# Performance work log

Hardware: AMD Instinct MI355X
Metric: run time of the kernel (lower is better)

Reference implementation:

```python
import jax, jax.numpy as jnp
import numpy as np

B, T, D = 4, 2048, 1024  # batch, seq, latent_dim == attn_dim
H = 16                   # n_heads
HS = D // H              # head_size = 64
FF = 4 * D               # ffn hidden
EPS = 1e-5


def layernorm(x, g, b):
    mu = jnp.mean(x, axis=-1, keepdims=True)
    var = jnp.mean(jnp.square(x - mu), axis=-1, keepdims=True)
    return (x - mu) * jax.lax.rsqrt(var + EPS) * g + b


def setup_inputs() -> dict:
    key = jax.random.key(0)
    ks = jax.random.split(key, 12)
    s = lambda fan_in: 1.0 / np.sqrt(fan_in)
    return {
        "x": jax.random.normal(ks[0], (B, T, D), dtype=jnp.float32),
        "ln1_g": jnp.ones((D,), jnp.float32),
        "ln1_b": jnp.zeros((D,), jnp.float32),
        "W_ap": jax.random.normal(ks[1], (D, D), jnp.float32) * s(D),
        "b_ap": jnp.zeros((D,), jnp.float32),
        "W_qkv": jax.random.normal(ks[2], (D, 3 * D), jnp.float32) * s(D),
        "b_qkv": jnp.zeros((3 * D,), jnp.float32),
        "W_proj": jax.random.normal(ks[3], (D, D), jnp.float32) * s(D),
        "b_proj": jnp.zeros((D,), jnp.float32),
        "ln2_g": jnp.ones((D,), jnp.float32),
        "ln2_b": jnp.zeros((D,), jnp.float32),
        "W1": jax.random.normal(ks[4], (D, FF), jnp.float32) * s(D),
        "b1": jnp.zeros((FF,), jnp.float32),
        "W2": jax.random.normal(ks[5], (FF, D), jnp.float32) * s(FF),
        "b2": jnp.zeros((D,), jnp.float32),
    }


def block_fwd(x, ln1_g, ln1_b, W_ap, b_ap, W_qkv, b_qkv, W_proj, b_proj,
              ln2_g, ln2_b, W1, b1, W2, b2):
    # --- self attention branch ---
    a = layernorm(x, ln1_g, ln1_b)
    a = a @ W_ap + b_ap                       # [B,T,D]
    qkv = a @ W_qkv + b_qkv                   # [B,T,3D]
    q, k, v = jnp.split(qkv, 3, axis=-1)
    q = q.reshape(B, T, H, HS).transpose(0, 2, 1, 3)  # [B,H,T,HS]
    k = k.reshape(B, T, H, HS).transpose(0, 2, 1, 3)
    v = v.reshape(B, T, H, HS).transpose(0, 2, 1, 3)
    scores = jnp.einsum('bhqd,bhkd->bhqk', q, k) * (1.0 / np.sqrt(HS))
    probs = jax.nn.softmax(scores, axis=-1)   # full [B,H,T,T], no causal mask (as in source)
    o = jnp.einsum('bhqk,bhkd->bhqd', probs, v)
    o = o.transpose(0, 2, 1, 3).reshape(B, T, D)
    o = o @ W_proj + b_proj
    h = x + o
    # --- ffn branch: GELU(LayerNorm(h)) -> Linear -> GELU -> Linear ---
    f = jax.nn.gelu(layernorm(h, ln2_g, ln2_b), approximate=False)
    f = jax.nn.gelu(f @ W1 + b1, approximate=False) @ W2 + b2
    return h + f


def reference(x, ln1_g, ln1_b, W_ap, b_ap, W_qkv, b_qkv, W_proj, b_proj,
              ln2_g, ln2_b, W1, b1, W2, b2):
    return block_fwd(x, ln1_g, ln1_b, W_ap, b_ap, W_qkv, b_qkv, W_proj, b_proj,
                     ln2_g, ln2_b, W1, b1, W2, b2)
```

## Files before the change

kernel.cpp:

```cpp
#include <hip/hip_runtime.h>
#include <hip/hip_bf16.h>
#include <math.h>


typedef unsigned short u16;
typedef __attribute__((ext_vector_type(8))) short s16x8;
typedef __attribute__((ext_vector_type(4))) float f32x4;

__device__ __forceinline__ u16 f2bf(float f) {
    unsigned u = __float_as_uint(f);
    u += 0x7fffu + ((u >> 16) & 1u);
    return (u16)(u >> 16);
}
__device__ __forceinline__ unsigned pkbf2(float a, float b) {
    float2 t; t.x = a; t.y = b;
    __hip_bfloat162 r = __float22bfloat162_rn(t);
    return *(unsigned*)&r;
}
__device__ __forceinline__ float bf2f(short s) {
    return __uint_as_float(((unsigned)(unsigned short)s) << 16);
}
__device__ __forceinline__ float gelu_f(float v) {
    float u = v * v;
    float x = v * fmaf(0.0356774081f, u, 0.7978845608f);
    float t = __builtin_amdgcn_exp2f(x * 2.885390082f);
    float th = fmaf(-2.0f, __builtin_amdgcn_rcpf(t + 1.0f), 1.0f);
    float hv = 0.5f * v;
    return fmaf(hv, th, hv);
}
__device__ __forceinline__ void glds16(const u16* g, u16* l) {
    __builtin_amdgcn_global_load_lds(
        (const __attribute__((address_space(1))) void*)g,
        (__attribute__((address_space(3))) void*)l, 16, 0, 0);
}
__device__ __forceinline__ void barfence() {
    __builtin_amdgcn_s_barrier();
    asm volatile("" ::: "memory");
}

__global__ __launch_bounds__(256) void transpose_f32_bf16(
    const float* __restrict__ in, u16* __restrict__ out, int K, int N) {
    __shared__ float t[32][33];
    int n0 = blockIdx.x * 32, k0 = blockIdx.y * 32;
    int c = threadIdx.x, r0 = threadIdx.y;
#pragma unroll
    for (int i = 0; i < 4; i++) {
        int r = r0 + i * 8;
        t[r][c] = in[(size_t)(k0 + r) * N + n0 + c];
    }
    __syncthreads();
#pragma unroll
    for (int i = 0; i < 4; i++) {
        int r = r0 + i * 8;
        out[(size_t)(n0 + r) * K + k0 + c] = f2bf(t[c][r]);
    }
}

template <bool GELU>
__global__ __launch_bounds__(256) void ln_kernel(
    const float* __restrict__ x, const float* __restrict__ g,
    const float* __restrict__ bt, u16* __restrict__ out) {
    const int D = 1024;
    int row = blockIdx.x;
    float4 v = reinterpret_cast<const float4*>(x + (size_t)row * D)[threadIdx.x];
    float s = v.x + v.y + v.z + v.w;
    float s2 = v.x * v.x + v.y * v.y + v.z * v.z + v.w * v.w;
#pragma unroll
    for (int off = 32; off > 0; off >>= 1) {
        s += __shfl_down(s, off);
        s2 += __shfl_down(s2, off);
    }
    __shared__ float red[8];
    int wid = threadIdx.x >> 6;
    if ((threadIdx.x & 63) == 0) { red[wid] = s; red[wid + 4] = s2; }
    __syncthreads();
    s = red[0] + red[1] + red[2] + red[3];
    s2 = red[4] + red[5] + red[6] + red[7];
    float mu = s * (1.0f / 1024.0f);
    float var = s2 * (1.0f / 1024.0f) - mu * mu;
    float rstd = rsqrtf(var + 1e-5f);
    float4 gg = reinterpret_cast<const float4*>(g)[threadIdx.x];
    float4 bb = reinterpret_cast<const float4*>(bt)[threadIdx.x];
    float o0 = (v.x - mu) * rstd * gg.x + bb.x;
    float o1 = (v.y - mu) * rstd * gg.y + bb.y;
    float o2 = (v.z - mu) * rstd * gg.z + bb.z;
    float o3 = (v.w - mu) * rstd * gg.w + bb.w;
    if (GELU) { o0 = gelu_f(o0); o1 = gelu_f(o1); o2 = gelu_f(o2); o3 = gelu_f(o3); }
    uint2 o;
    o.x = pkbf2(o0, o1); o.y = pkbf2(o2, o3);
    reinterpret_cast<uint2*>(out + (size_t)row * D)[threadIdx.x] = o;
}

template <int OUT_BF16, int ACT_GELU, int HAS_RES>
__global__ __launch_bounds__(512, 2) void gemm_kernel(
    const u16* __restrict__ A, const u16* __restrict__ BT,
    const float* __restrict__ bias, const float* __restrict__ res,
    void* __restrict__ outp, int M, int N, int K) {
    __shared__ u16 As[2 * 256 * 64];
    __shared__ u16 Bs[2 * 256 * 64];
    const int nwg = gridDim.x * gridDim.y;
    int wg = blockIdx.y * gridDim.x + blockIdx.x;
    wg = (wg & 7) * (nwg >> 3) + (wg >> 3);
    const int m0 = (wg / gridDim.x) * 256, n0 = (wg % gridDim.x) * 256;
    const int tid = threadIdx.x;
    const int w = tid >> 6, lane = tid & 63, l16 = lane & 15, quad = lane >> 4;
    const int wm = w >> 2, wn = w & 3;

    const int lrow = lane >> 3;
    const int lcol = ((lane & 7) ^ lrow) * 8;
    const u16* Ag = A + (size_t)(m0 + w * 16 + lrow) * K + lcol;
    const u16* Bg = BT + (size_t)(n0 + w * 16 + lrow) * K + lcol;

    const int cx0 = (quad ^ (l16 & 7)) * 8;
    const int cx1 = cx0 ^ 32;

    f32x4 acc[2][2][4][2] = {};
    const int nt = K >> 6;

#define STAGE_A(AH, BUF, KK)                                              \
    do {                                                                  \
        const u16* _s = Ag + (size_t)((AH) * 128) * K + (KK);             \
        u16* _d = As + (BUF) * 16384 + ((AH) * 128 + w * 16) * 64;        \
        glds16(_s, _d);                                                   \
        glds16(_s + (size_t)8 * K, _d + 512);                             \
    } while (0)
#define STAGE_B(BH, BUF, KK)                                              \
    do {                                                                  \
        const u16* _s = Bg + (size_t)((BH) * 128) * K + (KK);             \
        u16* _d = Bs + (BUF) * 16384 + ((BH) * 128 + w * 16) * 64;        \
        glds16(_s, _d);                                                   \
        glds16(_s + (size_t)8 * K, _d + 512);                             \
    } while (0)

    STAGE_A(0, 0, 0);
    STAGE_B(0, 0, 0);
    STAGE_B(1, 0, 0);
    STAGE_A(1, 0, 0);
    asm volatile("s_waitcnt vmcnt(0)" ::: "memory");
    barfence();

    s16x8 af0[4][2], af1[4][2], bfA[2][2], bfB[2][2];

    for (int t = 0; t < nt; ++t) {
        const int cur = t & 1, nxt = cur ^ 1;
        const int kk = (t + 1) << 6;
        const bool pre = (t + 1) < nt;
        const u16* Ab = As + cur * 16384;
        const u16* Bb = Bs + cur * 16384;

#pragma unroll
        for (int j = 0; j < 2; ++j) {
            const u16* p = Bb + (wn * 32 + j * 16 + l16) * 64;
            bfA[j][0] = *(const s16x8*)(p + cx0);
            bfA[j][1] = *(const s16x8*)(p + cx1);
        }
#pragma unroll
        for (int i = 0; i < 4; ++i) {
            const u16* p = Ab + (wm * 64 + i * 16 + l16) * 64;
            af0[i][0] = *(const s16x8*)(p + cx0);
            af0[i][1] = *(const s16x8*)(p + cx1);
        }
#pragma unroll
        for (int j = 0; j < 2; ++j) {
            const u16* p = Bb + (128 + wn * 32 + j * 16 + l16) * 64;
            bfB[j][0] = *(const s16x8*)(p + cx0);
            bfB[j][1] = *(const s16x8*)(p + cx1);
        }
#pragma unroll
        for (int i = 0; i < 4; ++i) {
            const u16* p = Ab + (128 + wm * 64 + i * 16 + l16) * 64;
            af1[i][0] = *(const s16x8*)(p + cx0);
            af1[i][1] = *(const s16x8*)(p + cx1);
        }
        if (pre) {
            STAGE_A(0, nxt, kk);
            STAGE_B(0, nxt, kk);
            STAGE_B(1, nxt, kk);
            STAGE_A(1, nxt, kk);
        }
        __builtin_amdgcn_s_setprio(1);
#pragma unroll
        for (int kd = 0; kd < 2; ++kd)
#pragma unroll
            for (int i = 0; i < 4; ++i)
#pragma unroll
                for (int j = 0; j < 2; ++j)
                    acc[0][0][i][j] = __builtin_amdgcn_mfma_f32_16x16x32_bf16(
                        af0[i][kd], bfA[j][kd], acc[0][0][i][j], 0, 0, 0);
#pragma unroll
        for (int kd = 0; kd < 2; ++kd)
#pragma unroll
            for (int i = 0; i < 4; ++i)
#pragma unroll
                for (int j = 0; j < 2; ++j)
                    acc[0][1][i][j] = __builtin_amdgcn_mfma_f32_16x16x32_bf16(
                        af0[i][kd], bfB[j][kd], acc[0][1][i][j], 0, 0, 0);
#pragma unroll
        for (int kd = 0; kd < 2; ++kd)
#pragma unroll
            for (int i = 0; i < 4; ++i)
#pragma unroll
                for (int j = 0; j < 2; ++j)
                    acc[1][1][i][j] = __builtin_amdgcn_mfma_f32_16x16x32_bf16(
                        af1[i][kd], bfB[j][kd], acc[1][1][i][j], 0, 0, 0);
#pragma unroll
        for (int kd = 0; kd < 2; ++kd)
#pragma unroll
            for (int i = 0; i < 4; ++i)
#pragma unroll
                for (int j = 0; j < 2; ++j)
                    acc[1][0][i][j] = __builtin_amdgcn_mfma_f32_16x16x32_bf16(
                        af1[i][kd], bfA[j][kd], acc[1][0][i][j], 0, 0, 0);
        __builtin_amdgcn_s_setprio(0);
        if (pre) {
            asm volatile("s_waitcnt vmcnt(0)" ::: "memory");
            barfence();
        }
    }
#undef STAGE_A
#undef STAGE_B

    float bv[2][2];
#pragma unroll
    for (int bh = 0; bh < 2; ++bh)
#pragma unroll
        for (int j = 0; j < 2; ++j)
            bv[bh][j] = bias[n0 + bh * 128 + wn * 32 + j * 16 + l16];

#pragma unroll
    for (int ah = 0; ah < 2; ++ah)
#pragma unroll
        for (int i = 0; i < 4; ++i) {
            int rowb = m0 + ah * 128 + wm * 64 + i * 16 + quad * 4;
#pragma unroll
            for (int bh = 0; bh < 2; ++bh)
#pragma unroll
                for (int j = 0; j < 2; ++j) {
                    int col = n0 + bh * 128 + wn * 32 + j * 16 + l16;
#pragma unroll
                    for (int r = 0; r < 4; ++r) {
                        float v = acc[ah][bh][i][j][r] + bv[bh][j];
                        if (ACT_GELU) v = gelu_f(v);
                        size_t idx = (size_t)(rowb + r) * N + col;
                        if (HAS_RES) v += res[idx];
                        if (OUT_BF16) ((u16*)outp)[idx] = f2bf(v);
                        else          ((float*)outp)[idx] = v;
                    }
                }
        }
}

template <int OUT_BF16, int HAS_RES, int SPLIT_V>
__global__ __launch_bounds__(512, 2) void gemm_n128(
    const u16* __restrict__ A, const u16* __restrict__ BT,
    const float* __restrict__ bias, const float* __restrict__ res,
    void* __restrict__ outp, u16* __restrict__ vtg, int M, int N, int K) {
    __shared__ u16 As[3 * 256 * 64];
    __shared__ u16 Bs[3 * 128 * 64];
    const int nwg = gridDim.x * gridDim.y;
    int wg = blockIdx.y * gridDim.x + blockIdx.x;
    wg = (wg & 7) * (nwg >> 3) + (wg >> 3);
    const int m0 = (wg / gridDim.x) * 256, n0 = (wg % gridDim.x) * 128;
    const int tid = threadIdx.x;
    const int w = tid >> 6, lane = tid & 63, l16 = lane & 15, quad = lane >> 4;
    const int wm = w >> 1, wn = w & 1;

    const int lrow = lane >> 3;
    const int lcol = ((lane & 7) ^ lrow) * 8;
    const u16* Ag = A + (size_t)(m0 + w * 16 + lrow) * K + lcol;
    const u16* Bg = BT + (size_t)(n0 + w * 16 + lrow) * K + lcol;

    const int cx0 = (quad ^ (l16 & 7)) * 8;
    const int cx1 = cx0 ^ 32;

    f32x4 acc[4][4] = {};
    const int nt = K >> 6;

#define NSTAGE_A(BUF, KK)                                                 \
    do {                                                                  \
        const u16* _s = Ag + (KK);                                        \
        u16* _d = As + (BUF) * 16384 + (w * 16) * 64;                     \
        glds16(_s, _d);                                                   \
        glds16(_s + (size_t)8 * K, _d + 512);                             \
        glds16(_s + (size_t)128 * K, _d + 8192);                          \
        glds16(_s + (size_t)136 * K, _d + 8192 + 512);                    \
    } while (0)
#define NSTAGE_B(BUF, KK)                                                 \
    do {                                                                  \
        const u16* _s = Bg + (KK);                                        \
        u16* _d = Bs + (BUF) * 8192 + (w * 16) * 64;                      \
        glds16(_s, _d);                                                   \
        glds16(_s + (size_t)8 * K, _d + 512);                             \
    } while (0)

    NSTAGE_A(0, 0);
    NSTAGE_B(0, 0);
    NSTAGE_A(1, 64);
    NSTAGE_B(1, 64);
    asm volatile("s_waitcnt vmcnt(6)" ::: "memory");
    barfence();

    s16x8 af[4][2], bfA[2][2], bfB[2][2];
    int cur = 0, b2 = 2;
    for (int t = 0; t < nt; ++t) {
        const bool pre2 = (t + 2) < nt;
        const u16* Ab = As + cur * 16384;
        const u16* Bb = Bs + cur * 8192;
        const int kk2 = (t + 2) << 6;

#pragma unroll
        for (int j = 0; j < 2; ++j) {
            const u16* p = Bb + (wn * 64 + j * 16 + l16) * 64;
            bfA[j][0] = *(const s16x8*)(p + cx0);
            bfA[j][1] = *(const s16x8*)(p + cx1);
        }
#pragma unroll
        for (int i = 0; i < 4; ++i) {
            const u16* p = Ab + (wm * 64 + i * 16 + l16) * 64;
            af[i][0] = *(const s16x8*)(p + cx0);
            af[i][1] = *(const s16x8*)(p + cx1);
        }
#pragma unroll
        for (int j = 0; j < 2; ++j) {
            const u16* p = Bb + (wn * 64 + 32 + j * 16 + l16) * 64;
            bfB[j][0] = *(const s16x8*)(p + cx0);
            bfB[j][1] = *(const s16x8*)(p + cx1);
        }
        if (pre2) {
            NSTAGE_A(b2, kk2);
            NSTAGE_B(b2, kk2);
        }
        __builtin_amdgcn_s_setprio(1);
#pragma unroll
        for (int kd = 0; kd < 2; ++kd)
#pragma unroll
            for (int i = 0; i < 4; ++i)
#pragma unroll
                for (int j = 0; j < 2; ++j)
                    acc[i][j] = __builtin_amdgcn_mfma_f32_16x16x32_bf16(
                        af[i][kd], bfA[j][kd], acc[i][j], 0, 0, 0);
#pragma unroll
        for (int kd = 0; kd < 2; ++kd)
#pragma unroll
            for (int i = 0; i < 4; ++i)
#pragma unroll
                for (int j = 0; j < 2; ++j)
                    acc[i][2 + j] = __builtin_amdgcn_mfma_f32_16x16x32_bf16(
                        af[i][kd], bfB[j][kd], acc[i][2 + j], 0, 0, 0);
        __builtin_amdgcn_s_setprio(0);
        if (pre2)               asm volatile("s_waitcnt vmcnt(6)" ::: "memory");
        else if (t + 1 < nt)    asm volatile("s_waitcnt vmcnt(0)" ::: "memory");
        if (t + 1 < nt) barfence();

        cur = (cur == 2) ? 0 : cur + 1;
        b2 = (b2 == 2) ? 0 : b2 + 1;
    }
#undef NSTAGE_A
#undef NSTAGE_B

    float bv[4];
#pragma unroll
    for (int j = 0; j < 4; ++j) bv[j] = bias[n0 + wn * 64 + j * 16 + l16];

    if (SPLIT_V && n0 >= 2048) {
#pragma unroll
        for (int i = 0; i < 4; ++i) {
            int rowb = m0 + wm * 64 + i * 16 + quad * 4;
            int bb = rowb >> 11, tt = rowb & 2047;
            int tp = (tt & ~63) | (tt & 0x23) | ((tt & 0x0C) << 1) | ((tt & 0x10) >> 2);
#pragma unroll
            for (int j = 0; j < 4; ++j) {
                int vcol = n0 + wn * 64 + j * 16 + l16 - 2048;
                uint2 pk;
                pk.x = pkbf2(acc[i][j][0] + bv[j], acc[i][j][1] + bv[j]);
                pk.y = pkbf2(acc[i][j][2] + bv[j], acc[i][j][3] + bv[j]);
                *(uint2*)&vtg[((size_t)bb * 1024 + vcol) * 2048 + tp] = pk;
            }
        }
    } else {
#pragma unroll
        for (int i = 0; i < 4; ++i) {
            int rowb = m0 + wm * 64 + i * 16 + quad * 4;
#pragma unroll
            for (int j = 0; j < 4; ++j) {
                int col = n0 + wn * 64 + j * 16 + l16;
#pragma unroll
                for (int r = 0; r < 4; ++r) {
                    float v = acc[i][j][r] + bv[j];
                    size_t idx = (size_t)(rowb + r) * N + col;
                    if (HAS_RES) v += res[idx];
                    if (OUT_BF16) ((u16*)outp)[idx] = f2bf(v);
                    else          ((float*)outp)[idx] = v;
                }
            }
        }
    }
}

__global__ __launch_bounds__(256) void knorm_kernel(
    const u16* __restrict__ qkv, float* __restrict__ maxkn) {
    const int T = 2048, D3 = 3072;
    int bh = blockIdx.x, b = bh >> 4, h = bh & 15;
    const u16* kg = qkv + (size_t)b * T * D3 + 1024 + h * 64;
    float mx = 0.f;
#pragma unroll
    for (int i = 0; i < 8; i++) {
        const u16* kp = kg + (size_t)(threadIdx.x + i * 256) * D3;
        float ss = 0.f;
#pragma unroll
        for (int c = 0; c < 8; c++) {
            s16x8 v = *(const s16x8*)(kp + c * 8);
#pragma unroll
            for (int j = 0; j < 8; j++) { float f = bf2f(v[j]); ss = fmaf(f, f, ss); }
        }
        mx = fmaxf(mx, ss);
    }
#pragma unroll
    for (int off = 32; off > 0; off >>= 1) mx = fmaxf(mx, __shfl_down(mx, off));
    __shared__ float red[4];
    if ((threadIdx.x & 63) == 0) red[threadIdx.x >> 6] = mx;
    __syncthreads();
    if (threadIdx.x == 0)
        maxkn[bh] = sqrtf(fmaxf(fmaxf(red[0], red[1]), fmaxf(red[2], red[3])));
}

__global__ __launch_bounds__(256, 4) void attn_kernel(
    const u16* __restrict__ qkv, const u16* __restrict__ vtg,
    const float* __restrict__ maxkn, u16* __restrict__ o) {
    const int T = 2048, D3 = 3072, Dm = 1024;
    const int bh = blockIdx.x, qb = blockIdx.y;
    const int b = bh >> 4, h = bh & 15;
    const int tid = threadIdx.x;
    const int w = tid >> 6, lane = tid & 63, l16 = lane & 15, quad = lane >> 4;
    const size_t tokbase = (size_t)b * T;
    const float s2 = 0.125f * 1.44269504088896f;

    __shared__ u16 Ks[2][64 * 64];
    __shared__ u16 Vts[2][64 * 64];

    s16x8 bq[2][2];
    float m2[2];
    const float kn = maxkn[bh];
#pragma unroll
    for (int qs = 0; qs < 2; qs++) {
        int qrow = qb * 128 + w * 32 + qs * 16 + l16;
        const u16* qp = qkv + (tokbase + qrow) * D3 + h * 64 + quad * 8;
        bq[qs][0] = *(const s16x8*)qp;
        bq[qs][1] = *(const s16x8*)(qp + 32);
        float ss = 0.f;
#pragma unroll
        for (int kd = 0; kd < 2; kd++)
#pragma unroll
            for (int j = 0; j < 8; j++) {
                float v = bf2f(bq[qs][kd][j]); ss = fmaf(v, v, ss);
            }
        ss += __shfl_xor(ss, 16);
        ss += __shfl_xor(ss, 32);
        m2[qs] = sqrtf(ss) * kn * s2;
    }

    f32x4 acc_ot[2][4] = {};
    float lp[2] = {0.f, 0.f};

    const int lr = lane >> 3;
    const int lcs = ((lane & 7) ^ lr) * 8;
    const u16* kgl = qkv + tokbase * D3 + 1024 + h * 64 + (size_t)(w * 16 + lr) * D3 + lcs;
    const u16* vgl = vtg + ((size_t)b * 1024 + h * 64 + w * 16 + lr) * T + lcs;

    const int cq0 = (quad ^ (l16 & 7)) * 8;
    const int cq1 = cq0 ^ 32;

#define ASTAGE(BUF, KT)                                                   \
    do {                                                                  \
        const u16* _k = kgl + (size_t)(KT) * 64 * D3;                     \
        glds16(_k, &Ks[BUF][(w * 16) * 64]);                              \
        glds16(_k + (size_t)8 * D3, &Ks[BUF][(w * 16 + 8) * 64]);         \
        const u16* _v = vgl + (KT) * 64;                                  \
        glds16(_v, &Vts[BUF][(w * 16) * 64]);                             \
        glds16(_v + (size_t)8 * T, &Vts[BUF][(w * 16 + 8) * 64]);         \
    } while (0)

    ASTAGE(0, 0);
    asm volatile("s_waitcnt vmcnt(0)" ::: "memory");
    barfence();

    for (int kt = 0; kt < 32; kt++) {
        const int cur = kt & 1;
        if (kt + 1 < 32) ASTAGE(cur ^ 1, kt + 1);

        f32x4 st[2][4] = {};
        __builtin_amdgcn_s_setprio(1);
#pragma unroll
        for (int kd = 0; kd < 2; kd++)
#pragma unroll
            for (int kb = 0; kb < 4; kb++) {
                s16x8 ak = *(const s16x8*)&Ks[cur][(kb * 16 + l16) * 64 + (kd ? cq1 : cq0)];
#pragma unroll
                for (int qs = 0; qs < 2; qs++)
                    st[qs][kb] = __builtin_amdgcn_mfma_f32_16x16x32_bf16(
                        ak, bq[qs][kd], st[qs][kb], 0, 0, 0);
            }
        __builtin_amdgcn_s_setprio(0);

        unsigned px[2][4], py[2][4];
#pragma unroll
        for (int qs = 0; qs < 2; qs++) {
            float acc_l = 0.f;
#pragma unroll
            for (int kb = 0; kb < 4; kb++) {
#pragma unroll
                for (int r = 0; r < 4; r++) {
                    float pv = __builtin_amdgcn_exp2f(fmaf(st[qs][kb][r], s2, -m2[qs]));
                    st[qs][kb][r] = pv;
                    acc_l += pv;
                }
                px[qs][kb] = pkbf2(st[qs][kb][0], st[qs][kb][1]);
                py[qs][kb] = pkbf2(st[qs][kb][2], st[qs][kb][3]);
            }
            lp[qs] += acc_l;
        }

#pragma unroll
        for (int kk = 0; kk < 2; kk++) {
            s16x8 bp[2];
#pragma unroll
            for (int qs = 0; qs < 2; qs++) {
                union { s16x8 v; unsigned u[4]; } bb;
                bb.u[0] = px[qs][2 * kk];
                bb.u[1] = py[qs][2 * kk];
                bb.u[2] = px[qs][2 * kk + 1];
                bb.u[3] = py[qs][2 * kk + 1];
                bp[qs] = bb.v;
            }
            __builtin_amdgcn_s_setprio(1);
#pragma unroll
            for (int dt = 0; dt < 4; dt++) {
                s16x8 av = *(const s16x8*)&Vts[cur][(dt * 16 + l16) * 64 + (kk ? cq1 : cq0)];
#pragma unroll
                for (int qs = 0; qs < 2; qs++)
                    acc_ot[qs][dt] = __builtin_amdgcn_mfma_f32_16x16x32_bf16(
                        av, bp[qs], acc_ot[qs][dt], 0, 0, 0);
            }
            __builtin_amdgcn_s_setprio(0);
        }

        if (kt + 1 < 32) asm volatile("s_waitcnt vmcnt(0)" ::: "memory");
        barfence();
    }
#undef ASTAGE

#pragma unroll
    for (int qs = 0; qs < 2; qs++) {
        float l = lp[qs];
        l += __shfl_xor(l, 16);
        l += __shfl_xor(l, 32);
        float inv = 1.0f / l;
        int token = qb * 128 + w * 32 + qs * 16 + l16;
#pragma unroll
        for (int dt = 0; dt < 4; dt++) {
            uint2 pk;
            pk.x = pkbf2(acc_ot[qs][dt][0] * inv, acc_ot[qs][dt][1] * inv);
            pk.y = pkbf2(acc_ot[qs][dt][2] * inv, acc_ot[qs][dt][3] * inv);
            *(uint2*)&o[(tokbase + token) * Dm + h * 64 + dt * 16 + quad * 4] = pk;
        }
    }
}

extern "C" void kernel_launch(void* const* d_in, const int* in_sizes, int n_in,
                              void* d_out, int out_size, void* d_ws, size_t ws_size,
                              hipStream_t stream) {
    const int M = 8192;
    const int D = 1024, D3 = 3072, FF = 4096;

    const float* x      = (const float*)d_in[0];
    const float* ln1_g  = (const float*)d_in[1];
    const float* ln1_b  = (const float*)d_in[2];
    const float* W_ap   = (const float*)d_in[3];
    const float* b_ap   = (const float*)d_in[4];
    const float* W_qkv  = (const float*)d_in[5];
    const float* b_qkv  = (const float*)d_in[6];
    const float* W_proj = (const float*)d_in[7];
    const float* b_proj = (const float*)d_in[8];
    const float* ln2_g  = (const float*)d_in[9];
    const float* ln2_b  = (const float*)d_in[10];
    const float* W1     = (const float*)d_in[11];
    const float* b1     = (const float*)d_in[12];
    const float* W2     = (const float*)d_in[13];
    const float* b2     = (const float*)d_in[14];

    char* p = (char*)d_ws;
    auto carve = [&](size_t bytes) { char* r = p; p += (bytes + 255) & ~(size_t)255; return r; };
    u16*   WapT   = (u16*)carve((size_t)D * D * 2);
    u16*   WqkvT  = (u16*)carve((size_t)D * D3 * 2);
    u16*   WprojT = (u16*)carve((size_t)D * D * 2);
    u16*   W1T    = (u16*)carve((size_t)D * FF * 2);
    u16*   W2T    = (u16*)carve((size_t)FF * D * 2);
    u16*   aln    = (u16*)carve((size_t)M * D * 2);
    u16*   a1     = (u16*)carve((size_t)M * D * 2);
    u16*   qkvb   = (u16*)carve((size_t)M * D3 * 2);
    float* hbuf   = (float*)carve((size_t)M * D * 4);
    u16*   f1     = (u16*)carve((size_t)M * FF * 2);
    float* maxkn  = (float*)carve(64 * 4);
    u16* gbuf = aln;
    u16* obuf = a1;
    u16* vtg  = f1;

    dim3 tb(32, 8);
    transpose_f32_bf16<<<dim3(D / 32, D / 32), tb, 0, stream>>>(W_ap, WapT, D, D);
    transpose_f32_bf16<<<dim3(D3 / 32, D / 32), tb, 0, stream>>>(W_qkv, WqkvT, D, D3);
    transpose_f32_bf16<<<dim3(D / 32, D / 32), tb, 0, stream>>>(W_proj, WprojT, D, D);
    transpose_f32_bf16<<<dim3(FF / 32, D / 32), tb, 0, stream>>>(W1, W1T, D, FF);
    transpose_f32_bf16<<<dim3(D / 32, FF / 32), tb, 0, stream>>>(W2, W2T, FF, D);

    ln_kernel<false><<<M, 256, 0, stream>>>(x, ln1_g, ln1_b, aln);
    gemm_n128<1, 0, 0><<<dim3(D / 128, M / 256), 512, 0, stream>>>(
        aln, WapT, b_ap, nullptr, a1, nullptr, M, D, D);
    gemm_n128<1, 0, 1><<<dim3(D3 / 128, M / 256), 512, 0, stream>>>(
        a1, WqkvT, b_qkv, nullptr, qkvb, vtg, M, D3, D);
    knorm_kernel<<<64, 256, 0, stream>>>(qkvb, maxkn);
    attn_kernel<<<dim3(64, 16), 256, 0, stream>>>(qkvb, vtg, maxkn, obuf);
    gemm_n128<0, 1, 0><<<dim3(D / 128, M / 256), 512, 0, stream>>>(
        obuf, WprojT, b_proj, x, hbuf, nullptr, M, D, D);
    ln_kernel<true><<<M, 256, 0, stream>>>(hbuf, ln2_g, ln2_b, gbuf);
    gemm_kernel<1, 1, 0><<<dim3(FF / 256, M / 256), 512, 0, stream>>>(
        gbuf, W1T, b1, nullptr, f1, M, FF, D);
    gemm_n128<0, 1, 0><<<dim3(D / 128, M / 256), 512, 0, stream>>>(
        f1, W2T, b2, hbuf, (float*)d_out, nullptr, M, D, FF);
}
```

Before: 534.0 us.

## Deepen 256x256 GEMM pipeline with interleaved staged loads and reuse for QKV

Restructures the 256x256 GEMM main loop so global-to-LDS loads for the next two k-tiles are issued in quarter pieces between the MFMA groups. Each piece is followed by partial vmcnt waits and barriers, replacing the single full wait per tile. A-fragment registers are reused across halves to cut register pressure. The kernel gains a SPLIT_V epilogue that writes V transposed, so the QKV projection now uses the 256-wide tile instead of the 128-wide kernel. This adds more barriers per iteration and tricky vmcnt accounting that could be wrong at the tail.

```diff
diff --git a/kernel.cpp b/kernel.cpp
--- a/kernel.cpp
+++ b/kernel.cpp
@@ -91,11 +91,11 @@
     reinterpret_cast<uint2*>(out + (size_t)row * D)[threadIdx.x] = o;
 }
 
-template <int OUT_BF16, int ACT_GELU, int HAS_RES>
-__global__ __launch_bounds__(512, 2) void gemm_kernel(
+template <int OUT_BF16, int ACT_GELU, int SPLIT_V>
+__global__ __launch_bounds__(512, 2) void gemm256(
     const u16* __restrict__ A, const u16* __restrict__ BT,
-    const float* __restrict__ bias, const float* __restrict__ res,
-    void* __restrict__ outp, int M, int N, int K) {
+    const float* __restrict__ bias, void* __restrict__ outp,
+    u16* __restrict__ vtg, int M, int N, int K) {
     __shared__ u16 As[2 * 256 * 64];
     __shared__ u16 Bs[2 * 256 * 64];
     const int nwg = gridDim.x * gridDim.y;
@@ -117,84 +117,98 @@
     f32x4 acc[2][2][4][2] = {};
     const int nt = K >> 6;
 
-#define STAGE_A(AH, BUF, KK)                                              \
+#define SA(C, H, KK)                                                      \
     do {                                                                  \
-        const u16* _s = Ag + (size_t)((AH) * 128) * K + (KK);             \
-        u16* _d = As + (BUF) * 16384 + ((AH) * 128 + w * 16) * 64;        \
+        const u16* _s = Ag + (size_t)((H) * 128) * K + (KK);              \
+        u16* _d = As + (C) * 16384 + ((H) * 128 + w * 16) * 64;           \
         glds16(_s, _d);                                                   \
         glds16(_s + (size_t)8 * K, _d + 512);                             \
     } while (0)
-#define STAGE_B(BH, BUF, KK)                                              \
+#define SB(C, H, KK)                                                      \
     do {                                                                  \
-        const u16* _s = Bg + (size_t)((BH) * 128) * K + (KK);             \
-        u16* _d = Bs + (BUF) * 16384 + ((BH) * 128 + w * 16) * 64;        \
+        const u16* _s = Bg + (size_t)((H) * 128) * K + (KK);              \
+        u16* _d = Bs + (C) * 16384 + ((H) * 128 + w * 16) * 64;           \
         glds16(_s, _d);                                                   \
         glds16(_s + (size_t)8 * K, _d + 512);                             \
     } while (0)
 
-    STAGE_A(0, 0, 0);
-    STAGE_B(0, 0, 0);
-    STAGE_B(1, 0, 0);
-    STAGE_A(1, 0, 0);
-    asm volatile("s_waitcnt vmcnt(0)" ::: "memory");
+    SA(0, 0, 0); SB(0, 0, 0); SB(0, 1, 0); SA(0, 1, 0);
+    SA(1, 0, 64); SB(1, 0, 64); SB(1, 1, 64);
+    asm volatile("s_waitcnt vmcnt(6)" ::: "memory");
     barfence();
 
-    s16x8 af0[4][2], af1[4][2], bfA[2][2], bfB[2][2];
+    s16x8 af[4][2], bfA[2][2], bfB[2][2];
 
     for (int t = 0; t < nt; ++t) {
         const int cur = t & 1, nxt = cur ^ 1;
-        const int kk = (t + 1) << 6;
-        const bool pre = (t + 1) < nt;
         const u16* Ab = As + cur * 16384;
         const u16* Bb = Bs + cur * 16384;
-
+        const int kk1 = (t + 1) << 6, kk2 = (t + 2) << 6;
+        const bool s1 = (t + 1) < nt, s2 = (t + 2) < nt;
+
+#pragma unroll
+        for (int i = 0; i < 4; ++i) {
+            const u16* p = Ab + (wm * 64 + i * 16 + l16) * 64;
+            af[i][0] = *(const s16x8*)(p + cx0);
+            af[i][1] = *(const s16x8*)(p + cx1);
+        }
 #pragma unroll
         for (int j = 0; j < 2; ++j) {
             const u16* p = Bb + (wn * 32 + j * 16 + l16) * 64;
             bfA[j][0] = *(const s16x8*)(p + cx0);
             bfA[j][1] = *(const s16x8*)(p + cx1);
         }
-#pragma unroll
-        for (int i = 0; i < 4; ++i) {
-            const u16* p = Ab + (wm * 64 + i * 16 + l16) * 64;
-            af0[i][0] = *(const s16x8*)(p + cx0);
-            af0[i][1] = *(const s16x8*)(p + cx1);
-        }
+        if (s1) SA(nxt, 1, kk1);
+        asm volatile("s_waitcnt lgkmcnt(0)" ::: "memory");
+        __builtin_amdgcn_sched_barrier(0);
+        __builtin_amdgcn_s_setprio(1);
+#pragma unroll
+        for (int kd = 0; kd < 2; ++kd)
+#pragma unroll
+            for (int i = 0; i < 4; ++i)
+#pragma unroll
+                for (int j = 0; j < 2; ++j)
+                    acc[0][0][i][j] = __builtin_amdgcn_mfma_f32_16x16x32_bf16(
+                        af[i][kd], bfA[j][kd], acc[0][0][i][j], 0, 0, 0);
+        __builtin_amdgcn_s_setprio(0);
+        if (t < nt - 1) asm volatile("s_waitcnt vmcnt(10)" ::: "memory");
+        else            asm volatile("s_waitcnt vmcnt(2)" ::: "memory");
+        barfence();
+
 #pragma unroll
         for (int j = 0; j < 2; ++j) {
             const u16* p = Bb + (128 + wn * 32 + j * 16 + l16) * 64;
             bfB[j][0] = *(const s16x8*)(p + cx0);
             bfB[j][1] = *(const s16x8*)(p + cx1);
         }
+        if (s2) SA(cur, 0, kk2);
+        asm volatile("s_waitcnt lgkmcnt(0)" ::: "memory");
+        __builtin_amdgcn_sched_barrier(0);
+        __builtin_amdgcn_s_setprio(1);
+#pragma unroll
+        for (int kd = 0; kd < 2; ++kd)
+#pragma unroll
+            for (int i = 0; i < 4; ++i)
+#pragma unroll
+                for (int j = 0; j < 2; ++j)
+                    acc[0][1][i][j] = __builtin_amdgcn_mfma_f32_16x16x32_bf16(
+                        af[i][kd], bfB[j][kd], acc[0][1][i][j], 0, 0, 0);
+        __builtin_amdgcn_s_setprio(0);
+        if (s2)      asm volatile("s_waitcnt vmcnt(10)" ::: "memory");
+        else if (s1) asm volatile("s_waitcnt vmcnt(8)" ::: "memory");
+        else         asm volatile("s_waitcnt vmcnt(0)" ::: "memory");
+        barfence();
+
 #pragma unroll
         for (int i = 0; i < 4; ++i) {
             const u16* p = Ab + (128 + wm * 64 + i * 16 + l16) * 64;
-            af1[i][0] = *(const s16x8*)(p + cx0);
-            af1[i][1] = *(const s16x8*)(p + cx1);
-        }
-        if (pre) {
-            STAGE_A(0, nxt, kk);
-            STAGE_B(0, nxt, kk);
-            STAGE_B(1, nxt, kk);
-            STAGE_A(1, nxt, kk);
-        }
+            af[i][0] = *(const s16x8*)(p + cx0);
+            af[i][1] = *(const s16x8*)(p + cx1);
+        }
+        if (s2) SB(cur, 0, kk2);
+        asm volatile("s_waitcnt lgkmcnt(0)" ::: "memory");
+        __builtin_amdgcn_sched_barrier(0);
         __builtin_amdgcn_s_setprio(1);
-#pragma unroll
-        for (int kd = 0; kd < 2; ++kd)
-#pragma unroll
-            for (int i = 0; i < 4; ++i)
-#pragma unroll
-                for (int j = 0; j < 2; ++j)
-                    acc[0][0][i][j] = __builtin_amdgcn_mfma_f32_16x16x32_bf16(
-                        af0[i][kd], bfA[j][kd], acc[0][0][i][j], 0, 0, 0);
-#pragma unroll
-        for (int kd = 0; kd < 2; ++kd)
-#pragma unroll
-            for (int i = 0; i < 4; ++i)
-#pragma unroll
-                for (int j = 0; j < 2; ++j)
-                    acc[0][1][i][j] = __builtin_amdgcn_mfma_f32_16x16x32_bf16(
-                        af0[i][kd], bfB[j][kd], acc[0][1][i][j], 0, 0, 0);
 #pragma unroll
         for (int kd = 0; kd < 2; ++kd)
 #pragma unroll
@@ -202,7 +216,11 @@
 #pragma unroll
                 for (int j = 0; j < 2; ++j)
                     acc[1][1][i][j] = __builtin_amdgcn_mfma_f32_16x16x32_bf16(
-                        af1[i][kd], bfB[j][kd], acc[1][1][i][j], 0, 0, 0);
+                        af[i][kd], bfB[j][kd], acc[1][1][i][j], 0, 0, 0);
+        __builtin_amdgcn_s_setprio(0);
+
+        if (s2) SB(cur, 1, kk2);
+        __builtin_amdgcn_s_setprio(1);
 #pragma unroll
         for (int kd = 0; kd < 2; ++kd)
 #pragma unroll
@@ -210,15 +228,18 @@
 #pragma unroll
                 for (int j = 0; j < 2; ++j)
                     acc[1][0][i][j] = __builtin_amdgcn_mfma_f32_16x16x32_bf16(
-                        af1[i][kd], bfA[j][kd], acc[1][0][i][j], 0, 0, 0);
+                        af[i][kd], bfA[j][kd], acc[1][0][i][j], 0, 0, 0);
         __builtin_amdgcn_s_setprio(0);
-        if (pre) {
-            asm volatile("s_waitcnt vmcnt(0)" ::: "memory");
+        if (s2) {
+            asm volatile("s_waitcnt vmcnt(10)" ::: "memory");
             barfence();
-        }
-    }
-#undef STAGE_A
-#undef STAGE_B
+        } else if (s1) {
+            asm volatile("s_waitcnt vmcnt(4)" ::: "memory");
+            barfence();
+        }
+    }
+#undef SA
+#undef SB
 
     float bv[2][2];
 #pragma unroll
@@ -227,27 +248,49 @@
         for (int j = 0; j < 2; ++j)
             bv[bh][j] = bias[n0 + bh * 128 + wn * 32 + j * 16 + l16];
 
-#pragma unroll
-    for (int ah = 0; ah < 2; ++ah)
-#pragma unroll
-        for (int i = 0; i < 4; ++i) {
-            int rowb = m0 + ah * 128 + wm * 64 + i * 16 + quad * 4;
-#pragma unroll
-            for (int bh = 0; bh < 2; ++bh)
-#pragma unroll
-                for (int j = 0; j < 2; ++j) {
-                    int col = n0 + bh * 128 + wn * 32 + j * 16 + l16;
-#pragma unroll
-                    for (int r = 0; r < 4; ++r) {
-                        float v = acc[ah][bh][i][j][r] + bv[bh][j];
-                        if (ACT_GELU) v = gelu_f(v);
-                        size_t idx = (size_t)(rowb + r) * N + col;
-                        if (HAS_RES) v += res[idx];
-                        if (OUT_BF16) ((u16*)outp)[idx] = f2bf(v);
-                        else          ((float*)outp)[idx] = v;
+    if (SPLIT_V && n0 >= 2048) {
+#pragma unroll
+        for (int ah = 0; ah < 2; ++ah)
+#pragma unroll
+            for (int i = 0; i < 4; ++i) {
+                int rowb = m0 + ah * 128 + wm * 64 + i * 16 + quad * 4;
+                int bb = rowb >> 11, tt = rowb & 2047;
+                int tp = (tt & ~63) | (tt & 0x23) | ((tt & 0x0C) << 1) | ((tt & 0x10) >> 2);
+#pragma unroll
+                for (int bh = 0; bh < 2; ++bh)
+#pragma unroll
+                    for (int j = 0; j < 2; ++j) {
+                        int vcol = n0 + bh * 128 + wn * 32 + j * 16 + l16 - 2048;
+                        uint2 pk;
+                        pk.x = pkbf2(acc[ah][bh][i][j][0] + bv[bh][j],
+                                     acc[ah][bh][i][j][1] + bv[bh][j]);
+                        pk.y = pkbf2(acc[ah][bh][i][j][2] + bv[bh][j],
+                                     acc[ah][bh][i][j][3] + bv[bh][j]);
+                        *(uint2*)&vtg[((size_t)bb * 1024 + vcol) * 2048 + tp] = pk;
                     }
-                }
-        }
+            }
+    } else {
+#pragma unroll
+        for (int ah = 0; ah < 2; ++ah)
+#pragma unroll
+            for (int i = 0; i < 4; ++i) {
+                int rowb = m0 + ah * 128 + wm * 64 + i * 16 + quad * 4;
+#pragma unroll
+                for (int bh = 0; bh < 2; ++bh)
+#pragma unroll
+                    for (int j = 0; j < 2; ++j) {
+                        int col = n0 + bh * 128 + wn * 32 + j * 16 + l16;
+#pragma unroll
+                        for (int r = 0; r < 4; ++r) {
+                            float v = acc[ah][bh][i][j][r] + bv[bh][j];
+                            if (ACT_GELU) v = gelu_f(v);
+                            size_t idx = (size_t)(rowb + r) * N + col;
+                            if (OUT_BF16) ((u16*)outp)[idx] = f2bf(v);
+                            else          ((float*)outp)[idx] = v;
+                        }
+                    }
+            }
+    }
 }
 
 template <int OUT_BF16, int HAS_RES, int SPLIT_V>
@@ -615,15 +658,15 @@
     ln_kernel<false><<<M, 256, 0, stream>>>(x, ln1_g, ln1_b, aln);
     gemm_n128<1, 0, 0><<<dim3(D / 128, M / 256), 512, 0, stream>>>(
         aln, WapT, b_ap, nullptr, a1, nullptr, M, D, D);
-    gemm_n128<1, 0, 1><<<dim3(D3 / 128, M / 256), 512, 0, stream>>>(
-        a1, WqkvT, b_qkv, nullptr, qkvb, vtg, M, D3, D);
+    gemm256<1, 0, 1><<<dim3(D3 / 256, M / 256), 512, 0, stream>>>(
+        a1, WqkvT, b_qkv, qkvb, vtg, M, D3, D);
     knorm_kernel<<<64, 256, 0, stream>>>(qkvb, maxkn);
     attn_kernel<<<dim3(64, 16), 256, 0, stream>>>(qkvb, vtg, maxkn, obuf);
     gemm_n128<0, 1, 0><<<dim3(D / 128, M / 256), 512, 0, stream>>>(
         obuf, WprojT, b_proj, x, hbuf, nullptr, M, D, D);
     ln_kernel<true><<<M, 256, 0, stream>>>(hbuf, ln2_g, ln2_b, gbuf);
-    gemm_kernel<1, 1, 0><<<dim3(FF / 256, M / 256), 512, 0, stream>>>(
-        gbuf, W1T, b1, nullptr, f1, M, FF, D);
+    gemm256<1, 1, 0><<<dim3(FF / 256, M / 256), 512, 0, stream>>>(
+        gbuf, W1T, b1, f1, nullptr, M, FF, D);
     gemm_n128<0, 1, 0><<<dim3(D / 128, M / 256), 512, 0, stream>>>(
         f1, W2T, b2, hbuf, (float*)d_out, nullptr, M, D, FF);
 }
```

New measurement: 518.2 us. 2.9% less time.
